# Performance work log

Measured on AMD Instinct MI355X. Metric: run time of the kernel, lower is better.

Reference implementation:

```python
import jax, jax.numpy as jnp
import numpy as np

M, T, D = 4, 8192, 64   # d = d_qk + 2 = 64; last channel is time
NLIN = 3                # n_layers=2 hidden linears + output linear


def setup_inputs() -> dict:
    key = jax.random.key(0)
    ks = jax.random.split(key, 7)
    X = jax.random.normal(ks[0], (M, T, D), dtype=jnp.float32)
    # last feature channel is a sorted timestamp per modality
    times = jnp.sort(jax.random.uniform(ks[1], (M, T), dtype=jnp.float32) * 100.0, axis=1)
    X = X.at[:, :, -1].set(times)
    s = 1.0 / np.sqrt(D).astype(np.float32)
    wq_w = jax.random.normal(ks[2], (NLIN, D, D), dtype=jnp.float32) * s
    wq_b = jax.random.normal(ks[3], (NLIN, D), dtype=jnp.float32) * 0.01
    wk_w = jax.random.normal(ks[4], (M, NLIN, D, D), dtype=jnp.float32) * s
    wk_b = jax.random.normal(ks[5], (M, NLIN, D), dtype=jnp.float32) * 0.01
    return {"X": X, "wq_w": wq_w, "wq_b": wq_b, "wk_w": wk_w, "wk_b": wk_b}


def mlp(x, W, b):
    # W: (NLIN, D, D), b: (NLIN, D); relu on all but the last linear
    for i in range(NLIN - 1):
        x = jax.nn.relu(x @ W[i] + b[i])
    return x @ W[-1] + b[-1]


def causal_dot_product(Q, K, V, t1, t2):
    # out[i] = Q[i] @ sum_{j: t2[j] <= t1[i]} K[j] (outer) V[j]
    S = jnp.cumsum(K[:, :, None] * V[:, None, :], axis=0)  # (T, D, D) prefix K^T V state
    idx = jnp.searchsorted(t2, t1, side="right") - 1       # last key with t2 <= t1[i]
    Sg = jnp.where((idx >= 0)[:, None, None], S[jnp.clip(idx, 0, T - 1)], 0.0)
    return jnp.einsum("td,tde->te", Q, Sg)                   # (T, D)


def reference(X, wq_w, wq_b, wk_w, wk_b):
    t1 = X[0, :, -1]               # query times from modality m1
    Q = mlp(X[0], wq_w, wq_b)      # (T, D)

    def per_modality(Xm, Wm, bm):
        K = mlp(Xm, Wm, bm)        # (T, D)
        V = Xm                     # V = X in original
        t2 = Xm[:, -1]
        return causal_dot_product(Q, K, V, t1, t2)

    Z = jax.vmap(per_modality)(X, wk_w, wk_b)  # (M, T, D) == Zout[0]
    yhat = Z.sum(0)[:, :2]                     # Zout.sum(1)[..., :2]
    return yhat[None]                          # (1, T, 2)
```

## Files before the change

kernel.cpp:

```cpp
#include <hip/hip_runtime.h>

#define TT 8192
#define DD 64
#define MODS 4
#define NCH 256
#define CH  32
#define QPB 8

typedef __attribute__((ext_vector_type(8))) short bf16x8;
typedef __attribute__((ext_vector_type(4))) float f32x4;

__device__ __forceinline__ unsigned f2bf1(float x) {
    unsigned u = __float_as_uint(x);
    return (u + 0x7FFFu + ((u >> 16) & 1u)) >> 16;
}
__device__ __forceinline__ unsigned packbf(float a, float b) {
    return f2bf1(a) | (f2bf1(b) << 16);
}

__device__ __forceinline__ void stage_w(const float* __restrict__ Wl,
                                        unsigned short* wb, int c, int dp0)
{
    #pragma unroll
    for (int it = 0; it < 8; ++it) {
        int dp = dp0 + 4 * it;
        float w0 = Wl[(2 * dp)     * DD + c];
        float w1 = Wl[(2 * dp + 1) * DD + c];
        *(unsigned*)&wb[c * 72 + 2 * dp] = packbf(w0, w1);
    }
}

__global__ __launch_bounds__(256)
void mlp_scan(const float* __restrict__ X,
              const float* __restrict__ wq_w, const float* __restrict__ wq_b,
              const float* __restrict__ wk_w, const float* __restrict__ wk_b,
              float* __restrict__ Q, float* __restrict__ Ctot,
              float* __restrict__ Crow, float* __restrict__ times)
{
    __shared__ unsigned short xbuf[4][16][72];
    __shared__ unsigned short wbuf[2][64][72];
    __shared__ float kbuf[64][68];
    __shared__ float2 vstash[64];

    const int job = blockIdx.y;
    const float *xin, *Wj, *Bias;
    if (job == 0) { xin = X; Wj = wq_w; Bias = wq_b; }
    else {
        const int m = job - 1;
        xin  = X    + (size_t)m * TT * DD;
        Wj   = wk_w + (size_t)m * 3 * DD * DD;
        Bias = wk_b + (size_t)m * 3 * DD;
    }

    const int t    = threadIdx.x;
    const int wv   = t >> 6;
    const int lane = t & 63;
    const int quad = lane >> 4;
    const int l15  = lane & 15;
    const int row0 = blockIdx.x * 64 + wv * 16;
    unsigned short* xb = &xbuf[wv][0][0];
    const int wc = t & 63, wdp0 = t >> 6;

    {
        const float4* src = (const float4*)(xin + (size_t)row0 * DD);
        #pragma unroll
        for (int k = 0; k < 4; ++k) {
            int f = lane + 64 * k;
            int r = f >> 4, c4 = (f & 15) << 2;
            float4 v = src[f];
            if (job > 0) {
                if ((f & 15) == 0)  vstash[wv * 16 + r] = make_float2(v.x, v.y);
                if ((f & 15) == 15) times[(size_t)(job - 1) * TT + row0 + r] = v.w;
            }
            uint2 p = make_uint2(packbf(v.x, v.y), packbf(v.z, v.w));
            *(uint2*)&xb[r * 72 + c4] = p;
        }
    }

    stage_w(Wj, &wbuf[0][0][0], wc, wdp0);

    #pragma unroll
    for (int l = 0; l < 3; ++l) {
        __syncthreads();
        const unsigned short* wb = &wbuf[l & 1][0][0];
        if (l < 2)
            stage_w(Wj + (size_t)(l + 1) * DD * DD, &wbuf[(l + 1) & 1][0][0], wc, wdp0);

        const float* Bl = Bias + l * DD;
        f32x4 acc[4];
        #pragma unroll
        for (int mt = 0; mt < 4; ++mt) {
            float4 b4 = *(const float4*)(Bl + 16 * mt + quad * 4);
            acc[mt][0] = b4.x; acc[mt][1] = b4.y; acc[mt][2] = b4.z; acc[mt][3] = b4.w;
        }

        bf16x8 xf[2];
        #pragma unroll
        for (int kt = 0; kt < 2; ++kt)
            xf[kt] = *(const bf16x8*)&xb[l15 * 72 + quad * 8 + kt * 32];

        #pragma unroll
        for (int mt = 0; mt < 4; ++mt) {
            #pragma unroll
            for (int kt = 0; kt < 2; ++kt) {
                bf16x8 wf = *(const bf16x8*)&wb[(16 * mt + l15) * 72 + quad * 8 + kt * 32];
                acc[mt] = __builtin_amdgcn_mfma_f32_16x16x32_bf16(wf, xf[kt], acc[mt], 0, 0, 0);
            }
        }

        if (l < 2) {
            #pragma unroll
            for (int mt = 0; mt < 4; ++mt) {
                float r0 = fmaxf(acc[mt][0], 0.f), r1 = fmaxf(acc[mt][1], 0.f);
                float r2 = fmaxf(acc[mt][2], 0.f), r3 = fmaxf(acc[mt][3], 0.f);
                uint2 p = make_uint2(packbf(r0, r1), packbf(r2, r3));
                *(uint2*)&xb[l15 * 72 + 16 * mt + quad * 4] = p;
            }
        } else {
            #pragma unroll
            for (int mt = 0; mt < 4; ++mt) {
                float4 v = make_float4(acc[mt][0], acc[mt][1], acc[mt][2], acc[mt][3]);
                if (job == 0)
                    *(float4*)(Q + (size_t)(row0 + l15) * DD + 16 * mt + quad * 4) = v;
                else
                    *(float4*)(&kbuf[wv * 16 + l15][16 * mt + quad * 4]) = v;
            }
        }
    }

    if (job > 0) {
        __syncthreads();
        const int m    = job - 1;
        const int chl  = t >> 7;
        const int tid2 = t & 127;
        const int d = tid2 & 63, e = tid2 >> 6;
        const int ch = blockIdx.x * 2 + chl;
        const size_t rbase = ((size_t)m * TT + (size_t)ch * CH) * 128 + tid2;
        float acc = 0.f;
        #pragma unroll
        for (int j = 0; j < 4; ++j) {
            #pragma unroll
            for (int s = 0; s < 8; ++s) {
                const int r  = j * 8 + s;
                const int rr = chl * 32 + r;
                float kv = kbuf[rr][d];
                float vv = e ? vstash[rr].y : vstash[rr].x;
                acc = fmaf(kv, vv, acc);
                Crow[rbase + (size_t)r * 128] = acc;
            }
        }
        Ctot[((size_t)m * NCH + ch) * 128 + tid2] = acc;
    }
}

__global__ __launch_bounds__(256)
void prefix_find(const float* __restrict__ Ctot, float* __restrict__ PreC,
                 const float* __restrict__ times, int* __restrict__ idx)
{
    const int b = blockIdx.x;
    if (b < MODS) {
        __shared__ float hs[128];
        const int sub = threadIdx.x >> 7, t = threadIdx.x & 127;
        const size_t base = ((size_t)b * NCH + (size_t)sub * 128) * 128 + t;

        float tot = 0.f;
        #pragma unroll 8
        for (int c = 0; c < 128; ++c)
            tot += Ctot[base + (size_t)c * 128];
        if (sub == 0) hs[t] = tot;
        __syncthreads();

        float run = sub ? hs[t] : 0.f;
        #pragma unroll 1
        for (int bb = 0; bb < 16; ++bb) {
            float v[8];
            #pragma unroll
            for (int i = 0; i < 8; ++i)
                v[i] = Ctot[base + (size_t)(bb * 8 + i) * 128];
            #pragma unroll
            for (int i = 0; i < 8; ++i) {
                PreC[base + (size_t)(bb * 8 + i) * 128] = run;
                run += v[i];
            }
        }
    } else {
        const int bb = b - MODS;
        const int m  = bb >> 5;
        const int q  = ((bb & 31) << 8) + threadIdx.x;
        const float t1 = times[q];
        const float* t2 = times + (size_t)m * TT;
        int lo = 0, hi = TT;
        #pragma unroll 1
        for (int s = 0; s < 13; ++s) {
            int mid = (lo + hi) >> 1;
            bool le = (t2[mid] <= t1);
            lo = le ? mid + 1 : lo;
            hi = le ? hi : mid;
        }
        idx[(size_t)m * TT + q] = lo - 1;
    }
}

__global__ __launch_bounds__(256)
void gather_kernel(const float* __restrict__ Q,
                   const float* __restrict__ Crow,
                   const float* __restrict__ PreC, const int* __restrict__ idx,
                   float* __restrict__ out)
{
    const int bx   = blockIdx.x;
    const int q0   = ((bx & 7) << 10) | ((bx >> 3) << 3);
    const int m    = threadIdx.x >> 6;
    const int lane = threadIdx.x & 63;

    __shared__ float red[QPB][MODS][2];

    const int* idxm = idx + (size_t)m * TT;
    #pragma unroll
    for (int u = 0; u < QPB; ++u) {
        const int q  = q0 + u;
        const int id = idxm[q];
        float a0 = 0.f, a1 = 0.f;
        if (id >= 0) {
            const float qv = Q[(size_t)q * DD + lane];
            const int cg = id >> 5;
            const float* P = PreC + ((size_t)(m * NCH + cg) << 7);
            const float* R = Crow + (((size_t)m * TT + id) << 7);
            float s0 = P[lane]      + R[lane];
            float s1 = P[64 + lane] + R[64 + lane];
            a0 = qv * s0;
            a1 = qv * s1;
        }
        #pragma unroll
        for (int off = 32; off > 0; off >>= 1) {
            a0 += __shfl_xor(a0, off, 64);
            a1 += __shfl_xor(a1, off, 64);
        }
        if (lane == 0) { red[u][m][0] = a0; red[u][m][1] = a1; }
    }
    __syncthreads();
    if (threadIdx.x < QPB * 2) {
        const int u = threadIdx.x >> 1, e = threadIdx.x & 1;
        out[((q0 + u) << 1) + e] =
            red[u][0][e] + red[u][1][e] + red[u][2][e] + red[u][3][e];
    }
}

extern "C" void kernel_launch(void* const* d_in, const int* in_sizes, int n_in,
                              void* d_out, int out_size, void* d_ws, size_t ws_size,
                              hipStream_t stream)
{
    const float* X    = (const float*)d_in[0];
    const float* wq_w = (const float*)d_in[1];
    const float* wq_b = (const float*)d_in[2];
    const float* wk_w = (const float*)d_in[3];
    const float* wk_b = (const float*)d_in[4];
    float* out = (float*)d_out;

    float* ws    = (float*)d_ws;
    float* Q     = ws;
    float* Crow  = Q     + (size_t)TT * DD;
    float* Ctot  = Crow  + (size_t)MODS * TT * 128;
    float* PreC  = Ctot  + (size_t)MODS * NCH * 128;
    float* times = PreC  + (size_t)MODS * NCH * 128;
    int*   idx   = (int*)(times + (size_t)MODS * TT);

    mlp_scan     <<<dim3(128, 5),  256, 0, stream>>>(X, wq_w, wq_b, wk_w, wk_b,
                                                     Q, Ctot, Crow, times);
    prefix_find  <<<MODS + 128,    256, 0, stream>>>(Ctot, PreC, times, idx);
    gather_kernel<<<TT / QPB,      256, 0, stream>>>(Q, Crow, PreC, idx, out);
}
```

Before: 91.76 us.

## Fuse chunk prefix into scan via last-block counter and move searchsorted into gather

Removes the separate prefix_find kernel. The cross-chunk prefix sum now runs in mlp_scan: an atomic counter lets the last block per modality detect completion and compute PreC. The per-query binary search moves into gather_kernel, using shared memory instead of a global idx array. This saves a kernel launch and an idx round-trip, but adds a memset, threadfence/atomic overhead and a serial tail where one block per modality does the whole prefix.

New measurement: 152.8 us. +66.5%, slower.

```diff
diff --git a/kernel.cpp b/kernel.cpp
--- a/kernel.cpp
+++ b/kernel.cpp
@@ -35,12 +35,15 @@
               const float* __restrict__ wq_w, const float* __restrict__ wq_b,
               const float* __restrict__ wk_w, const float* __restrict__ wk_b,
               float* __restrict__ Q, float* __restrict__ Ctot,
-              float* __restrict__ Crow, float* __restrict__ times)
+              float* __restrict__ Crow, float* __restrict__ PreC,
+              float* __restrict__ times, int* __restrict__ ctr)
 {
     __shared__ unsigned short xbuf[4][16][72];
     __shared__ unsigned short wbuf[2][64][72];
     __shared__ float kbuf[64][68];
     __shared__ float2 vstash[64];
+    __shared__ int   lastflag;
+    __shared__ float hs[128];
 
     const int job = blockIdx.y;
     const float *xin, *Wj, *Bias;
@@ -150,45 +153,58 @@
             }
         }
         Ctot[((size_t)m * NCH + ch) * 128 + tid2] = acc;
+
+        __threadfence();
+        __syncthreads();
+        if (t == 0)
+            lastflag = (atomicAdd(&ctr[m], 1) == gridDim.x - 1);
+        __syncthreads();
+        if (lastflag) {
+            __threadfence();
+            const int sub = t >> 7, tl = t & 127;
+            const size_t base = ((size_t)m * NCH + (size_t)sub * 128) * 128 + tl;
+
+            float tot = 0.f;
+            #pragma unroll 8
+            for (int c = 0; c < 128; ++c)
+                tot += Ctot[base + (size_t)c * 128];
+            if (sub == 0) hs[tl] = tot;
+            __syncthreads();
+
+            float run = sub ? hs[tl] : 0.f;
+            #pragma unroll 1
+            for (int bb = 0; bb < 16; ++bb) {
+                float v[8];
+                #pragma unroll
+                for (int i = 0; i < 8; ++i)
+                    v[i] = Ctot[base + (size_t)(bb * 8 + i) * 128];
+                #pragma unroll
+                for (int i = 0; i < 8; ++i) {
+                    PreC[base + (size_t)(bb * 8 + i) * 128] = run;
+                    run += v[i];
+                }
+            }
+        }
     }
 }
 
 __global__ __launch_bounds__(256)
-void prefix_find(const float* __restrict__ Ctot, float* __restrict__ PreC,
-                 const float* __restrict__ times, int* __restrict__ idx)
-{
-    const int b = blockIdx.x;
-    if (b < MODS) {
-        __shared__ float hs[128];
-        const int sub = threadIdx.x >> 7, t = threadIdx.x & 127;
-        const size_t base = ((size_t)b * NCH + (size_t)sub * 128) * 128 + t;
-
-        float tot = 0.f;
-        #pragma unroll 8
-        for (int c = 0; c < 128; ++c)
-            tot += Ctot[base + (size_t)c * 128];
-        if (sub == 0) hs[t] = tot;
-        __syncthreads();
-
-        float run = sub ? hs[t] : 0.f;
-        #pragma unroll 1
-        for (int bb = 0; bb < 16; ++bb) {
-            float v[8];
-            #pragma unroll
-            for (int i = 0; i < 8; ++i)
-                v[i] = Ctot[base + (size_t)(bb * 8 + i) * 128];
-            #pragma unroll
-            for (int i = 0; i < 8; ++i) {
-                PreC[base + (size_t)(bb * 8 + i) * 128] = run;
-                run += v[i];
-            }
-        }
-    } else {
-        const int bb = b - MODS;
-        const int m  = bb >> 5;
-        const int q  = ((bb & 31) << 8) + threadIdx.x;
-        const float t1 = times[q];
-        const float* t2 = times + (size_t)m * TT;
+void gather_kernel(const float* __restrict__ Q,
+                   const float* __restrict__ Crow,
+                   const float* __restrict__ PreC,
+                   const float* __restrict__ times,
+                   float* __restrict__ out)
+{
+    const int bx   = blockIdx.x;
+    const int q0   = ((bx & 7) << 10) | ((bx >> 3) << 3);
+
+    __shared__ int   idxs[QPB][MODS];
+    __shared__ float red[QPB][MODS][2];
+
+    if (threadIdx.x < QPB * MODS) {
+        const int u = threadIdx.x >> 2, mm = threadIdx.x & 3;
+        const float t1 = times[q0 + u];
+        const float* t2 = times + (size_t)mm * TT;
         int lo = 0, hi = TT;
         #pragma unroll 1
         for (int s = 0; s < 13; ++s) {
@@ -197,28 +213,17 @@
             lo = le ? mid + 1 : lo;
             hi = le ? hi : mid;
         }
-        idx[(size_t)m * TT + q] = lo - 1;
-    }
-}
-
-__global__ __launch_bounds__(256)
-void gather_kernel(const float* __restrict__ Q,
-                   const float* __restrict__ Crow,
-                   const float* __restrict__ PreC, const int* __restrict__ idx,
-                   float* __restrict__ out)
-{
-    const int bx   = blockIdx.x;
-    const int q0   = ((bx & 7) << 10) | ((bx >> 3) << 3);
+        idxs[u][mm] = lo - 1;
+    }
+    __syncthreads();
+
     const int m    = threadIdx.x >> 6;
     const int lane = threadIdx.x & 63;
 
-    __shared__ float red[QPB][MODS][2];
-
-    const int* idxm = idx + (size_t)m * TT;
     #pragma unroll
     for (int u = 0; u < QPB; ++u) {
         const int q  = q0 + u;
-        const int id = idxm[q];
+        const int id = idxs[u][m];
         float a0 = 0.f, a1 = 0.f;
         if (id >= 0) {
             const float qv = Q[(size_t)q * DD + lane];
@@ -262,10 +267,10 @@
     float* Ctot  = Crow  + (size_t)MODS * TT * 128;
     float* PreC  = Ctot  + (size_t)MODS * NCH * 128;
     float* times = PreC  + (size_t)MODS * NCH * 128;
-    int*   idx   = (int*)(times + (size_t)MODS * TT);
-
-    mlp_scan     <<<dim3(128, 5),  256, 0, stream>>>(X, wq_w, wq_b, wk_w, wk_b,
-                                                     Q, Ctot, Crow, times);
-    prefix_find  <<<MODS + 128,    256, 0, stream>>>(Ctot, PreC, times, idx);
-    gather_kernel<<<TT / QPB,      256, 0, stream>>>(Q, Crow, PreC, idx, out);
-}
+    int*   ctr   = (int*)(times + (size_t)MODS * TT);
+
+    hipMemsetAsync(ctr, 0, MODS * sizeof(int), stream);
+    mlp_scan     <<<dim3(128, 5), 256, 0, stream>>>(X, wq_w, wq_b, wk_w, wk_b,
+                                                    Q, Ctot, Crow, PreC, times, ctr);
+    gather_kernel<<<TT / QPB,     256, 0, stream>>>(Q, Crow, PreC, times, out);
+}
```
